# Kernel optimization log

Hardware: AMD Instinct MI355X
Metric: run time of the kernel (lower is better)

## Reference

```python
import jax, jax.numpy as jnp
import numpy as np

K, T, V = 64, 100, 10000
DELTA = 0.005
EPS_DIV = 1e-6


def setup_inputs() -> dict:
    key = jax.random.key(0)
    k1, k2, k3 = jax.random.split(key, 3)
    mu_q_beta = jax.random.normal(k1, (K, T, V), dtype=jnp.float32)
    logsig_q_beta = jax.random.normal(k2, (K, T, V), dtype=jnp.float32)
    eps = jax.random.normal(k3, (T, K, V), dtype=jnp.float32)  # randn_like noise for reparameterize
    return {"mu_q_beta": mu_q_beta, "logsig_q_beta": logsig_q_beta, "eps": eps}


def reference(mu_q_beta, logsig_q_beta, eps):
    # Rearrange params from [K, T, V] to the time-major layout [T, K, V]
    mu = jnp.transpose(mu_q_beta, (1, 0, 2))
    ls = jnp.transpose(logsig_q_beta, (1, 0, 2))

    # reparameterize: beta[t] = mu[t] + exp(0.5 * logsig[t]) * eps[t]
    # (beta[t] has no dependency on beta[t-1] -> fully vectorized over T)
    betas = mu + jnp.exp(0.5 * ls) * eps  # [T, K, V]

    # KL at t=0 against N(0, I): p_logsigma = 0 -> sigma_p_sq = 1
    kl0 = 0.5 * jnp.sum((jnp.exp(ls[0]) + mu[0] ** 2) / (1.0 + EPS_DIV) - 1.0 - ls[0])

    # KL at t>=1 against N(beta[t-1], delta): sigma_p_sq = delta, p_logsigma = log(delta)
    log_delta = jnp.log(jnp.float32(DELTA))
    diff = mu[1:] - betas[:-1]  # one-step lag prior mean
    kl_rest = 0.5 * jnp.sum(
        (jnp.exp(ls[1:]) + diff ** 2) / (DELTA + EPS_DIV) - 1.0 + log_delta - ls[1:]
    )

    kl_beta = kl0 + kl_rest
    return jax.nn.softmax(betas, axis=-1), kl_beta
```

## Files before the change

kernel.cpp:

```cpp
#include <hip/hip_runtime.h>
#include <math.h>

#define KDIM 64
#define TDIM 100
#define VDIM 10000
#define NV4  2500
#define BLOCK 256
#define NWAVE (BLOCK / 64)
#define VPT 10
#define HALF 5
#define CHUNK 5
#define NCHUNK (TDIM / CHUNK)

#define INV1 (1.0f / (1.0f + 1e-6f))
#define INVD (1.0f / (0.005f + 1e-6f))
#define LOGD (-5.2983173665480363f)

__device__ __forceinline__ float wave_red_sum(float v) {
#pragma unroll
    for (int m = 32; m >= 1; m >>= 1) v += __shfl_xor(v, m, 64);
    return v;
}

__device__ __forceinline__ void consume(const float4 m, const float4 l, const float4 e,
                                        float4& bp, const bool first,
                                        float& klacc, float& lsum) {
    float4 b;
    b.x = fmaf(__expf(0.5f * l.x), e.x, m.x);
    b.y = fmaf(__expf(0.5f * l.y), e.y, m.y);
    b.z = fmaf(__expf(0.5f * l.z), e.z, m.z);
    b.w = fmaf(__expf(0.5f * l.w), e.w, m.w);
    if (first) {
        klacc += (__expf(l.x) + m.x * m.x) * INV1 - 1.0f - l.x;
        klacc += (__expf(l.y) + m.y * m.y) * INV1 - 1.0f - l.y;
        klacc += (__expf(l.z) + m.z * m.z) * INV1 - 1.0f - l.z;
        klacc += (__expf(l.w) + m.w * m.w) * INV1 - 1.0f - l.w;
    } else {
        const float dx = m.x - bp.x, dy = m.y - bp.y, dz = m.z - bp.z, dw = m.w - bp.w;
        klacc += (__expf(l.x) + dx * dx) * INVD - 1.0f + LOGD - l.x;
        klacc += (__expf(l.y) + dy * dy) * INVD - 1.0f + LOGD - l.y;
        klacc += (__expf(l.z) + dz * dz) * INVD - 1.0f + LOGD - l.z;
        klacc += (__expf(l.w) + dw * dw) * INVD - 1.0f + LOGD - l.w;
    }
    bp = b;
    lsum += __expf(b.x) + __expf(b.y) + __expf(b.z) + __expf(b.w);
}

__global__ __launch_bounds__(BLOCK) void fused_beta_softmax_kl(
    const float* __restrict__ mu_q,
    const float* __restrict__ lsq,
    const float* __restrict__ eps,
    float* __restrict__ out,
    float* __restrict__ kl)
{
    __shared__ float red[2][NWAVE];
    __shared__ float kred[NWAVE];

    const int tid = threadIdx.x;
    const int bid = blockIdx.x;
    const int k   = bid / NCHUNK;
    const int c   = bid % NCHUNK;
    const int t0  = c * CHUNK;

    float4 bprev[VPT];
    float  klacc = 0.0f;

    float4 M[HALF], L[HALF], E[HALF];

    if (t0 > 0) {
        const size_t po = ((size_t)k * TDIM + (t0 - 1)) * VDIM;
        const size_t eo = ((size_t)(t0 - 1) * KDIM + k) * VDIM;
        const float4* m4p = reinterpret_cast<const float4*>(mu_q + po);
        const float4* l4p = reinterpret_cast<const float4*>(lsq + po);
        const float4* e4p = reinterpret_cast<const float4*>(eps + eo);
#pragma unroll
        for (int jj = 0; jj < HALF; ++jj) {
            const int idx = tid + jj * BLOCK;
            M[jj] = m4p[idx]; L[jj] = l4p[idx]; E[jj] = e4p[idx];
        }
#pragma unroll
        for (int jj = 0; jj < HALF; ++jj) {
            float4 b;
            b.x = fmaf(__expf(0.5f * L[jj].x), E[jj].x, M[jj].x);
            b.y = fmaf(__expf(0.5f * L[jj].y), E[jj].y, M[jj].y);
            b.z = fmaf(__expf(0.5f * L[jj].z), E[jj].z, M[jj].z);
            b.w = fmaf(__expf(0.5f * L[jj].w), E[jj].w, M[jj].w);
            bprev[jj] = b;
        }
#pragma unroll
        for (int jj = 0; jj < HALF; ++jj) {
            const int idx = tid + (HALF + jj) * BLOCK;
            if (idx < NV4) { M[jj] = m4p[idx]; L[jj] = l4p[idx]; E[jj] = e4p[idx]; }
        }
#pragma unroll
        for (int jj = 0; jj < HALF; ++jj) {
            const int idx = tid + (HALF + jj) * BLOCK;
            if (idx < NV4) {
                float4 b;
                b.x = fmaf(__expf(0.5f * L[jj].x), E[jj].x, M[jj].x);
                b.y = fmaf(__expf(0.5f * L[jj].y), E[jj].y, M[jj].y);
                b.z = fmaf(__expf(0.5f * L[jj].z), E[jj].z, M[jj].z);
                b.w = fmaf(__expf(0.5f * L[jj].w), E[jj].w, M[jj].w);
                bprev[HALF + jj] = b;
            }
        }
    }

    for (int t = t0; t < t0 + CHUNK; ++t) {
        const size_t po = ((size_t)k * TDIM + t) * VDIM;
        const size_t eo = ((size_t)t * KDIM + k) * VDIM;
        const float4* m4p = reinterpret_cast<const float4*>(mu_q + po);
        const float4* l4p = reinterpret_cast<const float4*>(lsq + po);
        const float4* e4p = reinterpret_cast<const float4*>(eps + eo);
        const bool first = (t == 0);

        float lsum = 0.0f;

#pragma unroll
        for (int jj = 0; jj < HALF; ++jj) {
            const int idx = tid + jj * BLOCK;
            M[jj] = m4p[idx]; L[jj] = l4p[idx]; E[jj] = e4p[idx];
        }
#pragma unroll
        for (int jj = 0; jj < HALF; ++jj)
            consume(M[jj], L[jj], E[jj], bprev[jj], first, klacc, lsum);

#pragma unroll
        for (int jj = 0; jj < HALF; ++jj) {
            const int idx = tid + (HALF + jj) * BLOCK;
            if (idx < NV4) { M[jj] = m4p[idx]; L[jj] = l4p[idx]; E[jj] = e4p[idx]; }
        }
#pragma unroll
        for (int jj = 0; jj < HALF; ++jj) {
            const int idx = tid + (HALF + jj) * BLOCK;
            if (idx < NV4)
                consume(M[jj], L[jj], E[jj], bprev[HALF + jj], first, klacc, lsum);
        }

        const int slot = t & 1;
        float ws = wave_red_sum(lsum);
        if ((tid & 63) == 0) red[slot][tid >> 6] = ws;
        __syncthreads();
        float rowsum = 0.0f;
#pragma unroll
        for (int w = 0; w < NWAVE; ++w) rowsum += red[slot][w];
        const float invs = 1.0f / rowsum;

        float4* o4p = reinterpret_cast<float4*>(out + ((size_t)t * KDIM + k) * VDIM);
#pragma unroll
        for (int j = 0; j < VPT; ++j) {
            const int idx = tid + j * BLOCK;
            if (idx < NV4) {
                const float4 b = bprev[j];
                float4 o;
                o.x = __expf(b.x) * invs;
                o.y = __expf(b.y) * invs;
                o.z = __expf(b.z) * invs;
                o.w = __expf(b.w) * invs;
                o4p[idx] = o;
            }
        }
    }

    float wk = wave_red_sum(klacc);
    __syncthreads();
    if ((tid & 63) == 0) kred[tid >> 6] = wk;
    __syncthreads();
    if (tid == 0) {
        float tot = 0.0f;
#pragma unroll
        for (int w = 0; w < NWAVE; ++w) tot += kred[w];
        atomicAdd(kl, 0.5f * tot);
    }
}

extern "C" void kernel_launch(void* const* d_in, const int* in_sizes, int n_in,
                              void* d_out, int out_size, void* d_ws, size_t ws_size,
                              hipStream_t stream) {
    const float* mu_q = (const float*)d_in[0];
    const float* lsq  = (const float*)d_in[1];
    const float* eps  = (const float*)d_in[2];
    float* out = (float*)d_out;
    float* kl  = out + (size_t)TDIM * KDIM * VDIM;

    hipMemsetAsync(kl, 0, sizeof(float), stream);

    dim3 grid(KDIM * NCHUNK);
    fused_beta_softmax_kl<<<grid, BLOCK, 0, stream>>>(mu_q, lsq, eps, out, kl);
}
```

Measured before the change: 238.9 us.

## Double-buffer timestep loads and move halo KL to chunk epilogue

```diff
diff --git a/kernel.cpp b/kernel.cpp
--- a/kernel.cpp
+++ b/kernel.cpp
@@ -22,31 +22,46 @@
     return v;
 }
 
+__device__ __forceinline__ void lds_barrier() {
+    asm volatile("s_waitcnt lgkmcnt(0)\n\ts_barrier" ::: "memory");
+}
+
 __device__ __forceinline__ void consume(const float4 m, const float4 l, const float4 e,
-                                        float4& bp, const bool first,
+                                        float4& bp, const bool first, const bool skip_kl,
                                         float& klacc, float& lsum) {
     float4 b;
     b.x = fmaf(__expf(0.5f * l.x), e.x, m.x);
     b.y = fmaf(__expf(0.5f * l.y), e.y, m.y);
     b.z = fmaf(__expf(0.5f * l.z), e.z, m.z);
     b.w = fmaf(__expf(0.5f * l.w), e.w, m.w);
-    if (first) {
-        klacc += (__expf(l.x) + m.x * m.x) * INV1 - 1.0f - l.x;
-        klacc += (__expf(l.y) + m.y * m.y) * INV1 - 1.0f - l.y;
-        klacc += (__expf(l.z) + m.z * m.z) * INV1 - 1.0f - l.z;
-        klacc += (__expf(l.w) + m.w * m.w) * INV1 - 1.0f - l.w;
-    } else {
-        const float dx = m.x - bp.x, dy = m.y - bp.y, dz = m.z - bp.z, dw = m.w - bp.w;
-        klacc += (__expf(l.x) + dx * dx) * INVD - 1.0f + LOGD - l.x;
-        klacc += (__expf(l.y) + dy * dy) * INVD - 1.0f + LOGD - l.y;
-        klacc += (__expf(l.z) + dz * dz) * INVD - 1.0f + LOGD - l.z;
-        klacc += (__expf(l.w) + dw * dw) * INVD - 1.0f + LOGD - l.w;
+    if (!skip_kl) {
+        if (first) {
+            klacc += (__expf(l.x) + m.x * m.x) * INV1 - 1.0f - l.x;
+            klacc += (__expf(l.y) + m.y * m.y) * INV1 - 1.0f - l.y;
+            klacc += (__expf(l.z) + m.z * m.z) * INV1 - 1.0f - l.z;
+            klacc += (__expf(l.w) + m.w * m.w) * INV1 - 1.0f - l.w;
+        } else {
+            const float dx = m.x - bp.x, dy = m.y - bp.y, dz = m.z - bp.z, dw = m.w - bp.w;
+            klacc += (__expf(l.x) + dx * dx) * INVD - 1.0f + LOGD - l.x;
+            klacc += (__expf(l.y) + dy * dy) * INVD - 1.0f + LOGD - l.y;
+            klacc += (__expf(l.z) + dz * dz) * INVD - 1.0f + LOGD - l.z;
+            klacc += (__expf(l.w) + dw * dw) * INVD - 1.0f + LOGD - l.w;
+        }
     }
     bp = b;
     lsum += __expf(b.x) + __expf(b.y) + __expf(b.z) + __expf(b.w);
 }
 
-__global__ __launch_bounds__(BLOCK) void fused_beta_softmax_kl(
+__device__ __forceinline__ void kl_step(const float4 m, const float4 l,
+                                        const float4 bp, float& klacc) {
+    const float dx = m.x - bp.x, dy = m.y - bp.y, dz = m.z - bp.z, dw = m.w - bp.w;
+    klacc += (__expf(l.x) + dx * dx) * INVD - 1.0f + LOGD - l.x;
+    klacc += (__expf(l.y) + dy * dy) * INVD - 1.0f + LOGD - l.y;
+    klacc += (__expf(l.z) + dz * dz) * INVD - 1.0f + LOGD - l.z;
+    klacc += (__expf(l.w) + dw * dw) * INVD - 1.0f + LOGD - l.w;
+}
+
+__global__ __launch_bounds__(BLOCK, 2) void fused_beta_softmax_kl(
     const float* __restrict__ mu_q,
     const float* __restrict__ lsq,
     const float* __restrict__ eps,
@@ -61,86 +76,97 @@
     const int k   = bid / NCHUNK;
     const int c   = bid % NCHUNK;
     const int t0  = c * CHUNK;
+    const int tend = t0 + CHUNK;
+    const bool epi = (tend < TDIM);
 
     float4 bprev[VPT];
     float  klacc = 0.0f;
-
-    float4 M[HALF], L[HALF], E[HALF];
-
-    if (t0 > 0) {
-        const size_t po = ((size_t)k * TDIM + (t0 - 1)) * VDIM;
-        const size_t eo = ((size_t)(t0 - 1) * KDIM + k) * VDIM;
+    float4 MA[HALF], LA[HALF], EA[HALF];
+    float4 MB[HALF], LB[HALF], EB[HALF];
+
+    {
+        const size_t po = ((size_t)k * TDIM + t0) * VDIM;
+        const size_t eo = ((size_t)t0 * KDIM + k) * VDIM;
         const float4* m4p = reinterpret_cast<const float4*>(mu_q + po);
         const float4* l4p = reinterpret_cast<const float4*>(lsq + po);
         const float4* e4p = reinterpret_cast<const float4*>(eps + eo);
 #pragma unroll
         for (int jj = 0; jj < HALF; ++jj) {
             const int idx = tid + jj * BLOCK;
-            M[jj] = m4p[idx]; L[jj] = l4p[idx]; E[jj] = e4p[idx];
-        }
-#pragma unroll
-        for (int jj = 0; jj < HALF; ++jj) {
-            float4 b;
-            b.x = fmaf(__expf(0.5f * L[jj].x), E[jj].x, M[jj].x);
-            b.y = fmaf(__expf(0.5f * L[jj].y), E[jj].y, M[jj].y);
-            b.z = fmaf(__expf(0.5f * L[jj].z), E[jj].z, M[jj].z);
-            b.w = fmaf(__expf(0.5f * L[jj].w), E[jj].w, M[jj].w);
-            bprev[jj] = b;
+            MA[jj] = m4p[idx]; LA[jj] = l4p[idx]; EA[jj] = e4p[idx];
         }
 #pragma unroll
         for (int jj = 0; jj < HALF; ++jj) {
             const int idx = tid + (HALF + jj) * BLOCK;
-            if (idx < NV4) { M[jj] = m4p[idx]; L[jj] = l4p[idx]; E[jj] = e4p[idx]; }
-        }
-#pragma unroll
-        for (int jj = 0; jj < HALF; ++jj) {
-            const int idx = tid + (HALF + jj) * BLOCK;
-            if (idx < NV4) {
-                float4 b;
-                b.x = fmaf(__expf(0.5f * L[jj].x), E[jj].x, M[jj].x);
-                b.y = fmaf(__expf(0.5f * L[jj].y), E[jj].y, M[jj].y);
-                b.z = fmaf(__expf(0.5f * L[jj].z), E[jj].z, M[jj].z);
-                b.w = fmaf(__expf(0.5f * L[jj].w), E[jj].w, M[jj].w);
-                bprev[HALF + jj] = b;
-            }
-        }
-    }
-
-    for (int t = t0; t < t0 + CHUNK; ++t) {
-        const size_t po = ((size_t)k * TDIM + t) * VDIM;
-        const size_t eo = ((size_t)t * KDIM + k) * VDIM;
-        const float4* m4p = reinterpret_cast<const float4*>(mu_q + po);
-        const float4* l4p = reinterpret_cast<const float4*>(lsq + po);
-        const float4* e4p = reinterpret_cast<const float4*>(eps + eo);
+            if (idx < NV4) { MB[jj] = m4p[idx]; LB[jj] = l4p[idx]; EB[jj] = e4p[idx]; }
+        }
+    }
+
+    for (int t = t0; t < tend; ++t) {
+        const int  tn    = t + 1;
         const bool first = (t == 0);
-
+        const bool skip  = (t == t0) && (t0 != 0);
         float lsum = 0.0f;
 
 #pragma unroll
-        for (int jj = 0; jj < HALF; ++jj) {
-            const int idx = tid + jj * BLOCK;
-            M[jj] = m4p[idx]; L[jj] = l4p[idx]; E[jj] = e4p[idx];
-        }
-#pragma unroll
         for (int jj = 0; jj < HALF; ++jj)
-            consume(M[jj], L[jj], E[jj], bprev[jj], first, klacc, lsum);
-
-#pragma unroll
-        for (int jj = 0; jj < HALF; ++jj) {
-            const int idx = tid + (HALF + jj) * BLOCK;
-            if (idx < NV4) { M[jj] = m4p[idx]; L[jj] = l4p[idx]; E[jj] = e4p[idx]; }
-        }
+            consume(MA[jj], LA[jj], EA[jj], bprev[jj], first, skip, klacc, lsum);
+
+        if (tn < tend) {
+            const size_t po = ((size_t)k * TDIM + tn) * VDIM;
+            const size_t eo = ((size_t)tn * KDIM + k) * VDIM;
+            const float4* m4p = reinterpret_cast<const float4*>(mu_q + po);
+            const float4* l4p = reinterpret_cast<const float4*>(lsq + po);
+            const float4* e4p = reinterpret_cast<const float4*>(eps + eo);
+#pragma unroll
+            for (int jj = 0; jj < HALF; ++jj) {
+                const int idx = tid + jj * BLOCK;
+                MA[jj] = m4p[idx]; LA[jj] = l4p[idx]; EA[jj] = e4p[idx];
+            }
+        } else if (epi) {
+            const size_t po = ((size_t)k * TDIM + tend) * VDIM;
+            const float4* m4p = reinterpret_cast<const float4*>(mu_q + po);
+            const float4* l4p = reinterpret_cast<const float4*>(lsq + po);
+#pragma unroll
+            for (int jj = 0; jj < HALF; ++jj) {
+                const int idx = tid + jj * BLOCK;
+                MA[jj] = m4p[idx]; LA[jj] = l4p[idx];
+            }
+        }
+
 #pragma unroll
         for (int jj = 0; jj < HALF; ++jj) {
             const int idx = tid + (HALF + jj) * BLOCK;
             if (idx < NV4)
-                consume(M[jj], L[jj], E[jj], bprev[HALF + jj], first, klacc, lsum);
+                consume(MB[jj], LB[jj], EB[jj], bprev[HALF + jj], first, skip, klacc, lsum);
+        }
+
+        if (tn < tend) {
+            const size_t po = ((size_t)k * TDIM + tn) * VDIM;
+            const size_t eo = ((size_t)tn * KDIM + k) * VDIM;
+            const float4* m4p = reinterpret_cast<const float4*>(mu_q + po);
+            const float4* l4p = reinterpret_cast<const float4*>(lsq + po);
+            const float4* e4p = reinterpret_cast<const float4*>(eps + eo);
+#pragma unroll
+            for (int jj = 0; jj < HALF; ++jj) {
+                const int idx = tid + (HALF + jj) * BLOCK;
+                if (idx < NV4) { MB[jj] = m4p[idx]; LB[jj] = l4p[idx]; EB[jj] = e4p[idx]; }
+            }
+        } else if (epi) {
+            const size_t po = ((size_t)k * TDIM + tend) * VDIM;
+            const float4* m4p = reinterpret_cast<const float4*>(mu_q + po);
+            const float4* l4p = reinterpret_cast<const float4*>(lsq + po);
+#pragma unroll
+            for (int jj = 0; jj < HALF; ++jj) {
+                const int idx = tid + (HALF + jj) * BLOCK;
+                if (idx < NV4) { MB[jj] = m4p[idx]; LB[jj] = l4p[idx]; }
+            }
         }
 
         const int slot = t & 1;
         float ws = wave_red_sum(lsum);
         if ((tid & 63) == 0) red[slot][tid >> 6] = ws;
-        __syncthreads();
+        lds_barrier();
         float rowsum = 0.0f;
 #pragma unroll
         for (int w = 0; w < NWAVE; ++w) rowsum += red[slot][w];
@@ -162,6 +188,18 @@
         }
     }
 
+    if (epi) {
+#pragma unroll
+        for (int jj = 0; jj < HALF; ++jj)
+            kl_step(MA[jj], LA[jj], bprev[jj], klacc);
+#pragma unroll
+        for (int jj = 0; jj < HALF; ++jj) {
+            const int idx = tid + (HALF + jj) * BLOCK;
+            if (idx < NV4)
+                kl_step(MB[jj], LB[jj], bprev[HALF + jj], klacc);
+        }
+    }
+
     float wk = wave_red_sum(klacc);
     __syncthreads();
     if ((tid & 63) == 0) kred[tid >> 6] = wk;
```

Result: slower. 244.5 us (+2.3%).

## Move beta history to LDS, assign halo KL to previous chunk, widen block

Applied to the files above, without the earlier changes.

```diff
diff --git a/kernel.cpp b/kernel.cpp
--- a/kernel.cpp
+++ b/kernel.cpp
@@ -5,10 +5,9 @@
 #define TDIM 100
 #define VDIM 10000
 #define NV4  2500
-#define BLOCK 256
+#define BLOCK 512
 #define NWAVE (BLOCK / 64)
-#define VPT 10
-#define HALF 5
+#define VPT 5
 #define CHUNK 5
 #define NCHUNK (TDIM / CHUNK)
 
@@ -16,34 +15,16 @@
 #define INVD (1.0f / (0.005f + 1e-6f))
 #define LOGD (-5.2983173665480363f)
 
+#define INRANGE(jj, idx) ((jj) < VPT - 1 || (idx) < NV4)
+
 __device__ __forceinline__ float wave_red_sum(float v) {
 #pragma unroll
     for (int m = 32; m >= 1; m >>= 1) v += __shfl_xor(v, m, 64);
     return v;
 }
 
-__device__ __forceinline__ void consume(const float4 m, const float4 l, const float4 e,
-                                        float4& bp, const bool first,
-                                        float& klacc, float& lsum) {
-    float4 b;
-    b.x = fmaf(__expf(0.5f * l.x), e.x, m.x);
-    b.y = fmaf(__expf(0.5f * l.y), e.y, m.y);
-    b.z = fmaf(__expf(0.5f * l.z), e.z, m.z);
-    b.w = fmaf(__expf(0.5f * l.w), e.w, m.w);
-    if (first) {
-        klacc += (__expf(l.x) + m.x * m.x) * INV1 - 1.0f - l.x;
-        klacc += (__expf(l.y) + m.y * m.y) * INV1 - 1.0f - l.y;
-        klacc += (__expf(l.z) + m.z * m.z) * INV1 - 1.0f - l.z;
-        klacc += (__expf(l.w) + m.w * m.w) * INV1 - 1.0f - l.w;
-    } else {
-        const float dx = m.x - bp.x, dy = m.y - bp.y, dz = m.z - bp.z, dw = m.w - bp.w;
-        klacc += (__expf(l.x) + dx * dx) * INVD - 1.0f + LOGD - l.x;
-        klacc += (__expf(l.y) + dy * dy) * INVD - 1.0f + LOGD - l.y;
-        klacc += (__expf(l.z) + dz * dz) * INVD - 1.0f + LOGD - l.z;
-        klacc += (__expf(l.w) + dw * dw) * INVD - 1.0f + LOGD - l.w;
-    }
-    bp = b;
-    lsum += __expf(b.x) + __expf(b.y) + __expf(b.z) + __expf(b.w);
+__device__ __forceinline__ void lds_barrier() {
+    asm volatile("s_waitcnt lgkmcnt(0)\n\ts_barrier" ::: "memory");
 }
 
 __global__ __launch_bounds__(BLOCK) void fused_beta_softmax_kl(
@@ -53,6 +34,7 @@
     float* __restrict__ out,
     float* __restrict__ kl)
 {
+    __shared__ float4 bprev[NV4];
     __shared__ float red[2][NWAVE];
     __shared__ float kred[NWAVE];
 
@@ -61,86 +43,61 @@
     const int k   = bid / NCHUNK;
     const int c   = bid % NCHUNK;
     const int t0  = c * CHUNK;
+    const int tend = t0 + CHUNK;
+    const bool epi = (tend < TDIM);
 
-    float4 bprev[VPT];
-    float  klacc = 0.0f;
+    float klacc = 0.0f;
+    float4 M[VPT], L[VPT], E[VPT];
 
-    float4 M[HALF], L[HALF], E[HALF];
-
-    if (t0 > 0) {
-        const size_t po = ((size_t)k * TDIM + (t0 - 1)) * VDIM;
-        const size_t eo = ((size_t)(t0 - 1) * KDIM + k) * VDIM;
-        const float4* m4p = reinterpret_cast<const float4*>(mu_q + po);
-        const float4* l4p = reinterpret_cast<const float4*>(lsq + po);
-        const float4* e4p = reinterpret_cast<const float4*>(eps + eo);
-#pragma unroll
-        for (int jj = 0; jj < HALF; ++jj) {
-            const int idx = tid + jj * BLOCK;
-            M[jj] = m4p[idx]; L[jj] = l4p[idx]; E[jj] = e4p[idx];
-        }
-#pragma unroll
-        for (int jj = 0; jj < HALF; ++jj) {
-            float4 b;
-            b.x = fmaf(__expf(0.5f * L[jj].x), E[jj].x, M[jj].x);
-            b.y = fmaf(__expf(0.5f * L[jj].y), E[jj].y, M[jj].y);
-            b.z = fmaf(__expf(0.5f * L[jj].z), E[jj].z, M[jj].z);
-            b.w = fmaf(__expf(0.5f * L[jj].w), E[jj].w, M[jj].w);
-            bprev[jj] = b;
-        }
-#pragma unroll
-        for (int jj = 0; jj < HALF; ++jj) {
-            const int idx = tid + (HALF + jj) * BLOCK;
-            if (idx < NV4) { M[jj] = m4p[idx]; L[jj] = l4p[idx]; E[jj] = e4p[idx]; }
-        }
-#pragma unroll
-        for (int jj = 0; jj < HALF; ++jj) {
-            const int idx = tid + (HALF + jj) * BLOCK;
-            if (idx < NV4) {
-                float4 b;
-                b.x = fmaf(__expf(0.5f * L[jj].x), E[jj].x, M[jj].x);
-                b.y = fmaf(__expf(0.5f * L[jj].y), E[jj].y, M[jj].y);
-                b.z = fmaf(__expf(0.5f * L[jj].z), E[jj].z, M[jj].z);
-                b.w = fmaf(__expf(0.5f * L[jj].w), E[jj].w, M[jj].w);
-                bprev[HALF + jj] = b;
-            }
-        }
-    }
-
-    for (int t = t0; t < t0 + CHUNK; ++t) {
+    for (int t = t0; t < tend; ++t) {
         const size_t po = ((size_t)k * TDIM + t) * VDIM;
         const size_t eo = ((size_t)t * KDIM + k) * VDIM;
         const float4* m4p = reinterpret_cast<const float4*>(mu_q + po);
         const float4* l4p = reinterpret_cast<const float4*>(lsq + po);
         const float4* e4p = reinterpret_cast<const float4*>(eps + eo);
         const bool first = (t == 0);
+        const bool skip  = (t == t0) && (t0 != 0);
+
+#pragma unroll
+        for (int jj = 0; jj < VPT; ++jj) {
+            const int idx = tid + jj * BLOCK;
+            if (INRANGE(jj, idx)) { M[jj] = m4p[idx]; L[jj] = l4p[idx]; E[jj] = e4p[idx]; }
+        }
 
         float lsum = 0.0f;
-
 #pragma unroll
-        for (int jj = 0; jj < HALF; ++jj) {
+        for (int jj = 0; jj < VPT; ++jj) {
             const int idx = tid + jj * BLOCK;
-            M[jj] = m4p[idx]; L[jj] = l4p[idx]; E[jj] = e4p[idx];
-        }
-#pragma unroll
-        for (int jj = 0; jj < HALF; ++jj)
-            consume(M[jj], L[jj], E[jj], bprev[jj], first, klacc, lsum);
-
-#pragma unroll
-        for (int jj = 0; jj < HALF; ++jj) {
-            const int idx = tid + (HALF + jj) * BLOCK;
-            if (idx < NV4) { M[jj] = m4p[idx]; L[jj] = l4p[idx]; E[jj] = e4p[idx]; }
-        }
-#pragma unroll
-        for (int jj = 0; jj < HALF; ++jj) {
-            const int idx = tid + (HALF + jj) * BLOCK;
-            if (idx < NV4)
-                consume(M[jj], L[jj], E[jj], bprev[HALF + jj], first, klacc, lsum);
+            if (INRANGE(jj, idx)) {
+                const float4 m = M[jj], l = L[jj], e = E[jj];
+                float4 b;
+                b.x = fmaf(__expf(0.5f * l.x), e.x, m.x);
+                b.y = fmaf(__expf(0.5f * l.y), e.y, m.y);
+                b.z = fmaf(__expf(0.5f * l.z), e.z, m.z);
+                b.w = fmaf(__expf(0.5f * l.w), e.w, m.w);
+                if (first) {
+                    klacc += (__expf(l.x) + m.x * m.x) * INV1 - 1.0f - l.x;
+                    klacc += (__expf(l.y) + m.y * m.y) * INV1 - 1.0f - l.y;
+                    klacc += (__expf(l.z) + m.z * m.z) * INV1 - 1.0f - l.z;
+                    klacc += (__expf(l.w) + m.w * m.w) * INV1 - 1.0f - l.w;
+                } else if (!skip) {
+                    const float4 p = bprev[idx];
+                    const float dx = m.x - p.x, dy = m.y - p.y,
+                                dz = m.z - p.z, dw = m.w - p.w;
+                    klacc += (__expf(l.x) + dx * dx) * INVD - 1.0f + LOGD - l.x;
+                    klacc += (__expf(l.y) + dy * dy) * INVD - 1.0f + LOGD - l.y;
+                    klacc += (__expf(l.z) + dz * dz) * INVD - 1.0f + LOGD - l.z;
+                    klacc += (__expf(l.w) + dw * dw) * INVD - 1.0f + LOGD - l.w;
+                }
+                bprev[idx] = b;
+                lsum += __expf(b.x) + __expf(b.y) + __expf(b.z) + __expf(b.w);
+            }
         }
 
         const int slot = t & 1;
         float ws = wave_red_sum(lsum);
         if ((tid & 63) == 0) red[slot][tid >> 6] = ws;
-        __syncthreads();
+        lds_barrier();
         float rowsum = 0.0f;
 #pragma unroll
         for (int w = 0; w < NWAVE; ++w) rowsum += red[slot][w];
@@ -148,16 +105,41 @@
 
         float4* o4p = reinterpret_cast<float4*>(out + ((size_t)t * KDIM + k) * VDIM);
 #pragma unroll
-        for (int j = 0; j < VPT; ++j) {
-            const int idx = tid + j * BLOCK;
-            if (idx < NV4) {
-                const float4 b = bprev[j];
+        for (int jj = 0; jj < VPT; ++jj) {
+            const int idx = tid + jj * BLOCK;
+            if (INRANGE(jj, idx)) {
+                const float4 b = bprev[idx];
                 float4 o;
                 o.x = __expf(b.x) * invs;
                 o.y = __expf(b.y) * invs;
                 o.z = __expf(b.z) * invs;
                 o.w = __expf(b.w) * invs;
                 o4p[idx] = o;
+            }
+        }
+    }
+
+    if (epi) {
+        const size_t po = ((size_t)k * TDIM + tend) * VDIM;
+        const float4* m4p = reinterpret_cast<const float4*>(mu_q + po);
+        const float4* l4p = reinterpret_cast<const float4*>(lsq + po);
+#pragma unroll
+        for (int jj = 0; jj < VPT; ++jj) {
+            const int idx = tid + jj * BLOCK;
+            if (INRANGE(jj, idx)) { M[jj] = m4p[idx]; L[jj] = l4p[idx]; }
+        }
+#pragma unroll
+        for (int jj = 0; jj < VPT; ++jj) {
+            const int idx = tid + jj * BLOCK;
+            if (INRANGE(jj, idx)) {
+                const float4 m = M[jj], l = L[jj];
+                const float4 p = bprev[idx];
+                const float dx = m.x - p.x, dy = m.y - p.y,
+                            dz = m.z - p.z, dw = m.w - p.w;
+                klacc += (__expf(l.x) + dx * dx) * INVD - 1.0f + LOGD - l.x;
+                klacc += (__expf(l.y) + dy * dy) * INVD - 1.0f + LOGD - l.y;
+                klacc += (__expf(l.z) + dz * dz) * INVD - 1.0f + LOGD - l.z;
+                klacc += (__expf(l.w) + dw * dw) * INVD - 1.0f + LOGD - l.w;
             }
         }
     }
```

Result: faster. 228.1 us (-4.5%).
